# Performance work log

Measured on AMD Instinct MI355X. Metric: run time of the kernel, lower is better.

## Reference

```python
import jax, jax.numpy as jnp
import numpy as np


def _dequantize(qweight, scale, zero_point, bits, group_size):
    """Unpack int32-packed weights and apply group-wise dequantization.

    qweight:    [N, K // (32//bits)] int32, value i within an int32 at shift i*bits
    scale/zp:   [N, K // group_size]
    returns W:  [N, K] float32
    """
    vpi = 32 // bits  # values per int32
    mask = (1 << bits) - 1
    N, packed = qweight.shape
    K = packed * vpi
    shifts = (jnp.arange(vpi, dtype=jnp.int32) * bits)  # [vpi]
    # [N, packed, vpi] -> flatten so value i of each int32 lands at consecutive K positions
    q = (qweight[:, :, None] >> shifts[None, None, :]) & mask
    q = q.reshape(N, K // group_size, group_size).astype(jnp.float32)
    w = scale[:, :, None] * (q - zero_point[:, :, None])  # group-wise dequant
    return w.reshape(N, K)


def setup_inputs() -> dict:
    key = jax.random.key(0)
    k1, k2, k3, k4, k5 = jax.random.split(key, 5)
    B, S, K, N = 4, 2048, 4096, 4096
    bits, group_size = 4, 128
    vpi = 32 // bits
    num_groups = K // group_size
    x = jax.random.normal(k1, (B, S, K), dtype=jnp.float32)
    qweight = jax.random.randint(k2, (N, K // vpi), jnp.iinfo(jnp.int32).min,
                                 jnp.iinfo(jnp.int32).max, dtype=jnp.int32)
    scale = jax.random.uniform(k3, (N, num_groups), dtype=jnp.float32,
                               minval=0.001, maxval=0.02)
    zero_point = jax.random.uniform(k4, (N, num_groups), dtype=jnp.float32,
                                    minval=0.0, maxval=float((1 << bits) - 1))
    bias = jax.random.normal(k5, (N,), dtype=jnp.float32)
    return {"x": x, "qweight": qweight, "scale": scale, "zero_point": zero_point,
            "bias": bias, "bits": bits, "group_size": group_size}


def reference(x, qweight, scale, zero_point, bias, bits, group_size):
    # Fused dequant + GEMM: y = x @ W^T + b, W dequantized from packed int4 groups
    w = _dequantize(qweight, scale, zero_point, bits, group_size)  # [N, K]
    y = jnp.einsum('bsk,nk->bsn', x, w)
    return y + bias
```

## Files before the change

### kernel.cpp

```cpp
#include <hip/hip_runtime.h>

#define KD 4096
#define ND 4096
#define GRP 32

typedef unsigned short u16;
typedef float   f32x4  __attribute__((ext_vector_type(4)));
typedef __bf16  bf16x8 __attribute__((ext_vector_type(8)));
typedef unsigned short u16x8 __attribute__((ext_vector_type(8)));
typedef unsigned short u16x4 __attribute__((ext_vector_type(4)));

__device__ __forceinline__ u16 f2bf(float f) {
  unsigned u = __float_as_uint(f);
  return (u16)((u + 0x7fffu + ((u >> 16) & 1u)) >> 16);
}

__device__ __forceinline__ void async16(const void* g, void* l) {
  __builtin_amdgcn_global_load_lds(
      (const __attribute__((address_space(1))) unsigned int*)g,
      (__attribute__((address_space(3))) unsigned int*)l, 16, 0, 0);
}

__global__ __launch_bounds__(256) void prep_kernel(
    const int* __restrict__ qw, const float* __restrict__ scale,
    const float* __restrict__ zp, u16* __restrict__ wout,
    const float4* __restrict__ x, u16x4* __restrict__ xb) {
  const int b = blockIdx.x, tid = threadIdx.x;
  if (b < 8192) {
    int idx = b * 256 + tid;
    int n = idx >> 9;
    int p = idx & 511;
    int g = p >> 4;
    float s = scale[n * GRP + g];
    float bz = -s * zp[n * GRP + g];
    unsigned q = (unsigned)qw[idx];
    u16x8 hv;
#pragma unroll
    for (int i = 0; i < 8; ++i)
      hv[i] = f2bf(fmaf((float)((q >> (4 * i)) & 15u), s, bz));
    *(u16x8*)(wout + (size_t)idx * 8) = hv;
  } else {
    size_t i = (size_t)(b - 8192) * 256 + tid;
    float4 v = x[i];
    u16x4 h;
    h[0] = f2bf(v.x); h[1] = f2bf(v.y); h[2] = f2bf(v.z); h[3] = f2bf(v.w);
    xb[i] = h;
  }
}

template <int XF32, int WQ>
__global__ __launch_bounds__(256, 3) void gemm_kernel(
    const u16*   __restrict__ xb,
    const float* __restrict__ xf,
    const u16*   __restrict__ wb,
    const int*   __restrict__ qw,
    const float* __restrict__ scale,
    const float* __restrict__ zp,
    const float* __restrict__ bias,
    float* __restrict__ out) {
  __shared__ u16 As[128 * 64];
  __shared__ u16 Bs[128 * 64];
  const int tid = threadIdx.x;
  const int l = tid & 63, w = tid >> 6;
  const int m0 = blockIdx.y * 128, n0 = blockIdx.x * 128;
  const int wm = (w >> 1) * 64, wn = (w & 1) * 64;
  const int col = l & 15, quad = l >> 4;
  const int rsw = col & 7;
  const int lr = l >> 3;
  const int csrc = (l & 7) ^ lr;
  f32x4 acc[4][4] = {};

  for (int k0 = 0; k0 < KD; k0 += 64) {
    __syncthreads();

    if constexpr (XF32) {
#pragma unroll
      for (int it = 0; it < 8; ++it) {
        int fi = it * 256 + tid;
        int row = fi >> 4, cs = fi & 15;
        float4 v = *(const float4*)(xf + (size_t)(m0 + row) * KD + k0 + cs * 4);
        u16x4 h;
        h[0] = f2bf(v.x); h[1] = f2bf(v.y); h[2] = f2bf(v.z); h[3] = f2bf(v.w);
        int slot = (cs >> 1) ^ (row & 7);
        *(u16x4*)(&As[row * 64 + slot * 8 + (cs & 1) * 4]) = h;
      }
    } else {
#pragma unroll
      for (int c = 0; c < 4; ++c) {
        int br = w * 32 + c * 8;
        const u16* g = xb + (size_t)(m0 + br + lr) * KD + k0 + csrc * 8;
        async16(g, &As[br * 64]);
      }
    }

    if constexpr (WQ) {
#pragma unroll
      for (int it = 0; it < 4; ++it) {
        int qi = it * 256 + tid;
        int row = qi >> 3, p8 = qi & 7;
        int nrow = n0 + row;
        int g = k0 >> 7;
        float s = scale[nrow * GRP + g];
        float bz = -s * zp[nrow * GRP + g];
        unsigned q = (unsigned)qw[(size_t)nrow * (KD / 8) + (k0 >> 3) + p8];
        u16x8 hv;
#pragma unroll
        for (int i = 0; i < 8; ++i)
          hv[i] = f2bf(fmaf((float)((q >> (4 * i)) & 15u), s, bz));
        *(u16x8*)(&Bs[row * 64 + ((p8 ^ (row & 7)) * 8)]) = hv;
      }
    } else {
#pragma unroll
      for (int c = 0; c < 4; ++c) {
        int br = w * 32 + c * 8;
        const u16* g = wb + (size_t)(n0 + br + lr) * KD + k0 + csrc * 8;
        async16(g, &Bs[br * 64]);
      }
    }

    __syncthreads();

#pragma unroll
    for (int kk = 0; kk < 2; ++kk) {
      bf16x8 a[4], b[4];
      const int slot = ((kk * 4 + quad) ^ rsw) * 8;
#pragma unroll
      for (int i = 0; i < 4; ++i)
        a[i] = *(const bf16x8*)&As[(wm + i * 16 + col) * 64 + slot];
#pragma unroll
      for (int j = 0; j < 4; ++j)
        b[j] = *(const bf16x8*)&Bs[(wn + j * 16 + col) * 64 + slot];
#pragma unroll
      for (int i = 0; i < 4; ++i)
#pragma unroll
        for (int j = 0; j < 4; ++j)
          acc[i][j] = __builtin_amdgcn_mfma_f32_16x16x32_bf16(a[i], b[j], acc[i][j], 0, 0, 0);
    }
  }

#pragma unroll
  for (int j = 0; j < 4; ++j) {
    int n = n0 + wn + j * 16 + col;
    float bj = bias[n];
#pragma unroll
    for (int i = 0; i < 4; ++i) {
      int mrow = m0 + wm + i * 16 + quad * 4;
#pragma unroll
      for (int r = 0; r < 4; ++r)
        out[(size_t)(mrow + r) * ND + n] = acc[i][j][r] + bj;
    }
  }
}

extern "C" void kernel_launch(void* const* d_in, const int* in_sizes, int n_in,
                              void* d_out, int out_size, void* d_ws, size_t ws_size,
                              hipStream_t stream) {
  const float* x     = (const float*)d_in[0];
  const int*   qw    = (const int*)d_in[1];
  const float* scale = (const float*)d_in[2];
  const float* zp    = (const float*)d_in[3];
  const float* bias  = (const float*)d_in[4];
  float* out = (float*)d_out;

  const int M = in_sizes[0] / KD;
  dim3 grid(ND / 128, M / 128), block(256);

  const size_t needW = (size_t)ND * KD * sizeof(u16);
  const size_t needX = (size_t)M * KD * sizeof(u16);

  if (ws_size >= needW + needX) {
    u16* wb = (u16*)d_ws;
    u16* xb = wb + (size_t)ND * KD;
    int conv_blocks = (M * (KD / 4)) / 256;
    prep_kernel<<<8192 + conv_blocks, 256, 0, stream>>>(
        qw, scale, zp, wb, (const float4*)x, (u16x4*)xb);
    gemm_kernel<0, 0><<<grid, block, 0, stream>>>(xb, x, wb, qw, scale, zp, bias, out);
  } else if (ws_size >= needW) {
    u16* wb = (u16*)d_ws;
    prep_kernel<<<8192, 256, 0, stream>>>(qw, scale, zp, wb, nullptr, nullptr);
    gemm_kernel<1, 0><<<grid, block, 0, stream>>>(nullptr, x, wb, qw, scale, zp, bias, out);
  } else {
    gemm_kernel<1, 1><<<grid, block, 0, stream>>>(nullptr, x, nullptr, qw, scale, zp, bias, out);
  }
}
```

Baseline: 460.2 us.

## Add 256x256 double-buffered GEMM with XCD-aware block remap and grid-stride prep

```diff
diff --git a/kernel.cpp b/kernel.cpp
--- a/kernel.cpp
+++ b/kernel.cpp
@@ -3,6 +3,7 @@
 #define KD 4096
 #define ND 4096
 #define GRP 32
+#define NT (KD / 64)
 
 typedef unsigned short u16;
 typedef float   f32x4  __attribute__((ext_vector_type(4)));
@@ -24,10 +25,10 @@
 __global__ __launch_bounds__(256) void prep_kernel(
     const int* __restrict__ qw, const float* __restrict__ scale,
     const float* __restrict__ zp, u16* __restrict__ wout,
-    const float4* __restrict__ x, u16x4* __restrict__ xb) {
-  const int b = blockIdx.x, tid = threadIdx.x;
-  if (b < 8192) {
-    int idx = b * 256 + tid;
+    const float4* __restrict__ x, u16x4* __restrict__ xb, int nx) {
+  const int nth = gridDim.x * 256;
+  const int t0 = blockIdx.x * 256 + threadIdx.x;
+  for (int idx = t0; idx < ND * (KD / 8); idx += nth) {
     int n = idx >> 9;
     int p = idx & 511;
     int g = p >> 4;
@@ -39,8 +40,8 @@
     for (int i = 0; i < 8; ++i)
       hv[i] = f2bf(fmaf((float)((q >> (4 * i)) & 15u), s, bz));
     *(u16x8*)(wout + (size_t)idx * 8) = hv;
-  } else {
-    size_t i = (size_t)(b - 8192) * 256 + tid;
+  }
+  for (int i = t0; i < nx; i += nth) {
     float4 v = x[i];
     u16x4 h;
     h[0] = f2bf(v.x); h[1] = f2bf(v.y); h[2] = f2bf(v.z); h[3] = f2bf(v.w);
@@ -48,11 +49,156 @@
   }
 }
 
+__global__ __launch_bounds__(512, 2) void gemm256(
+    const u16* __restrict__ xb, const u16* __restrict__ wb,
+    const float* __restrict__ bias, float* __restrict__ out) {
+  __shared__ u16 As[2][256 * 64];
+  __shared__ u16 Bs[2][256 * 64];
+  const int tid = threadIdx.x;
+  const int l = tid & 63, w = tid >> 6;
+  const int wr = w >> 2, wc = w & 3;
+  const int col = l & 15, quad = l >> 4, rsw = col & 7;
+  const int lr = l >> 3, csrc = (l & 7) ^ lr;
+
+  const int id = blockIdx.y * gridDim.x + blockIdx.x;
+  const int nwg = gridDim.x * gridDim.y;
+  const int q = nwg >> 3, r = nwg & 7;
+  const int xcd = id & 7, off = id >> 3;
+  const int wgid = (xcd < r ? xcd * (q + 1) : r * (q + 1) + (xcd - r) * q) + off;
+  const int nb = gridDim.x;
+  const int m0 = (wgid / nb) * 256;
+  const int n0 = (wgid % nb) * 256;
+
+  const u16* asrc = xb + (size_t)(m0 + w * 16 + lr) * KD + csrc * 8;
+  const u16* bsrc = wb + (size_t)(n0 + w * 16 + lr) * KD + csrc * 8;
+
+#define STAGE_A(t, h)                                                      \
+  do {                                                                     \
+    const u16* _g = asrc + (size_t)((h) * 128) * KD + (t) * 64;            \
+    u16* _l = &As[(t) & 1][((h) * 128 + w * 16) * 64];                     \
+    async16(_g, _l);                                                       \
+    async16(_g + (size_t)8 * KD, _l + 8 * 64);                             \
+  } while (0)
+#define STAGE_B(t, h)                                                      \
+  do {                                                                     \
+    const u16* _g = bsrc + (size_t)((h) * 128) * KD + (t) * 64;            \
+    u16* _l = &Bs[(t) & 1][((h) * 128 + w * 16) * 64];                     \
+    async16(_g, _l);                                                       \
+    async16(_g + (size_t)8 * KD, _l + 8 * 64);                             \
+  } while (0)
+#define BAR()    asm volatile("s_barrier" ::: "memory")
+#define LGKM0()  asm volatile("s_waitcnt lgkmcnt(0)" ::: "memory")
+#define VMCNT2() asm volatile("s_waitcnt vmcnt(2)" ::: "memory")
+#define VMCNT0() asm volatile("s_waitcnt vmcnt(0)" ::: "memory")
+#define LDA(Ab, i, kk) \
+  (*(const bf16x8*)&(Ab)[(wr * 128 + (i) * 16 + col) * 64 + ((((kk) * 4 + quad) ^ rsw) * 8)])
+#define LDB(Bb, j, kk) \
+  (*(const bf16x8*)&(Bb)[(wc * 64 + (j) * 16 + col) * 64 + ((((kk) * 4 + quad) ^ rsw) * 8)])
+
+  f32x4 acc[8][4] = {};
+  bf16x8 a[4][2], b[4][2];
+
+  STAGE_A(0, 0); STAGE_A(0, 1); STAGE_B(0, 0); STAGE_B(0, 1);
+  STAGE_A(1, 0);
+  VMCNT2();
+  BAR();
+
+  for (int t = 0; t < NT; ++t) {
+    const u16* Ab = As[t & 1];
+    const u16* Bb = Bs[t & 1];
+
+#pragma unroll
+    for (int i = 0; i < 4; ++i) { a[i][0] = LDA(Ab, i, 0); a[i][1] = LDA(Ab, i, 1); }
+#pragma unroll
+    for (int j = 0; j < 2; ++j) { b[j][0] = LDB(Bb, j, 0); b[j][1] = LDB(Bb, j, 1); }
+    if (t + 1 < NT) STAGE_A(t + 1, 1);
+    BAR();
+    LGKM0();
+    __builtin_amdgcn_s_setprio(1);
+#pragma unroll
+    for (int kk = 0; kk < 2; ++kk)
+#pragma unroll
+      for (int i = 0; i < 4; ++i)
+#pragma unroll
+        for (int j = 0; j < 2; ++j)
+          acc[i][j] = __builtin_amdgcn_mfma_f32_16x16x32_bf16(a[i][kk], b[j][kk], acc[i][j], 0, 0, 0);
+    __builtin_amdgcn_s_setprio(0);
+    BAR();
+
+#pragma unroll
+    for (int j = 2; j < 4; ++j) { b[j][0] = LDB(Bb, j, 0); b[j][1] = LDB(Bb, j, 1); }
+    if (t + 1 < NT) STAGE_B(t + 1, 0);
+    BAR();
+    LGKM0();
+    __builtin_amdgcn_s_setprio(1);
+#pragma unroll
+    for (int kk = 0; kk < 2; ++kk)
+#pragma unroll
+      for (int i = 0; i < 4; ++i)
+#pragma unroll
+        for (int j = 2; j < 4; ++j)
+          acc[i][j] = __builtin_amdgcn_mfma_f32_16x16x32_bf16(a[i][kk], b[j][kk], acc[i][j], 0, 0, 0);
+    __builtin_amdgcn_s_setprio(0);
+    BAR();
+
+#pragma unroll
+    for (int i = 0; i < 4; ++i) { a[i][0] = LDA(Ab, i + 4, 0); a[i][1] = LDA(Ab, i + 4, 1); }
+    if (t + 1 < NT) STAGE_B(t + 1, 1);
+    BAR();
+    LGKM0();
+    __builtin_amdgcn_s_setprio(1);
+#pragma unroll
+    for (int kk = 0; kk < 2; ++kk)
+#pragma unroll
+      for (int i = 0; i < 4; ++i)
+#pragma unroll
+        for (int j = 0; j < 2; ++j)
+          acc[4 + i][j] = __builtin_amdgcn_mfma_f32_16x16x32_bf16(a[i][kk], b[j][kk], acc[4 + i][j], 0, 0, 0);
+    __builtin_amdgcn_s_setprio(0);
+    BAR();
+
+    if (t + 2 < NT) STAGE_A(t + 2, 0);
+    BAR();
+    __builtin_amdgcn_s_setprio(1);
+#pragma unroll
+    for (int kk = 0; kk < 2; ++kk)
+#pragma unroll
+      for (int i = 0; i < 4; ++i)
+#pragma unroll
+        for (int j = 2; j < 4; ++j)
+          acc[4 + i][j] = __builtin_amdgcn_mfma_f32_16x16x32_bf16(a[i][kk], b[j][kk], acc[4 + i][j], 0, 0, 0);
+    __builtin_amdgcn_s_setprio(0);
+    if (t + 2 < NT) VMCNT2(); else VMCNT0();
+    BAR();
+  }
+
+#pragma unroll
+  for (int j = 0; j < 4; ++j) {
+    int n = n0 + wc * 64 + j * 16 + col;
+    float bj = bias[n];
+#pragma unroll
+    for (int i = 0; i < 8; ++i) {
+      int mrow = m0 + wr * 128 + i * 16 + quad * 4;
+#pragma unroll
+      for (int rr = 0; rr < 4; ++rr)
+        out[(size_t)(mrow + rr) * ND + n] = acc[i][j][rr] + bj;
+    }
+  }
+#undef STAGE_A
+#undef STAGE_B
+#undef BAR
+#undef LGKM0
+#undef VMCNT2
+#undef VMCNT0
+#undef LDA
+#undef LDB
+}
+
 template <int XF32, int WQ>
 __global__ __launch_bounds__(256, 3) void gemm_kernel(
-    const u16*   __restrict__ xb,
+    const u16*   __restrict__ xbp,
     const float* __restrict__ xf,
-    const u16*   __restrict__ wb,
+    const u16*   __restrict__ wbp,
     const int*   __restrict__ qw,
     const float* __restrict__ scale,
     const float* __restrict__ zp,
@@ -88,7 +234,7 @@
 #pragma unroll
       for (int c = 0; c < 4; ++c) {
         int br = w * 32 + c * 8;
-        const u16* g = xb + (size_t)(m0 + br + lr) * KD + k0 + csrc * 8;
+        const u16* g = xbp + (size_t)(m0 + br + lr) * KD + k0 + csrc * 8;
         async16(g, &As[br * 64]);
       }
     }
@@ -102,18 +248,18 @@
         int g = k0 >> 7;
         float s = scale[nrow * GRP + g];
         float bz = -s * zp[nrow * GRP + g];
-        unsigned q = (unsigned)qw[(size_t)nrow * (KD / 8) + (k0 >> 3) + p8];
+        unsigned qv = (unsigned)qw[(size_t)nrow * (KD / 8) + (k0 >> 3) + p8];
         u16x8 hv;
 #pragma unroll
         for (int i = 0; i < 8; ++i)
-          hv[i] = f2bf(fmaf((float)((q >> (4 * i)) & 15u), s, bz));
+          hv[i] = f2bf(fmaf((float)((qv >> (4 * i)) & 15u), s, bz));
         *(u16x8*)(&Bs[row * 64 + ((p8 ^ (row & 7)) * 8)]) = hv;
       }
     } else {
 #pragma unroll
       for (int c = 0; c < 4; ++c) {
         int br = w * 32 + c * 8;
-        const u16* g = wb + (size_t)(n0 + br + lr) * KD + k0 + csrc * 8;
+        const u16* g = wbp + (size_t)(n0 + br + lr) * KD + k0 + csrc * 8;
         async16(g, &Bs[br * 64]);
       }
     }
@@ -146,8 +292,8 @@
     for (int i = 0; i < 4; ++i) {
       int mrow = m0 + wm + i * 16 + quad * 4;
 #pragma unroll
-      for (int r = 0; r < 4; ++r)
-        out[(size_t)(mrow + r) * ND + n] = acc[i][j][r] + bj;
+      for (int rr = 0; rr < 4; ++rr)
+        out[(size_t)(mrow + rr) * ND + n] = acc[i][j][rr] + bj;
     }
   }
 }
@@ -163,23 +309,25 @@
   float* out = (float*)d_out;
 
   const int M = in_sizes[0] / KD;
-  dim3 grid(ND / 128, M / 128), block(256);
 
   const size_t needW = (size_t)ND * KD * sizeof(u16);
   const size_t needX = (size_t)M * KD * sizeof(u16);
 
-  if (ws_size >= needW + needX) {
+  if (ws_size >= needW + needX && (M % 256) == 0) {
     u16* wb = (u16*)d_ws;
-    u16* xb = wb + (size_t)ND * KD;
-    int conv_blocks = (M * (KD / 4)) / 256;
-    prep_kernel<<<8192 + conv_blocks, 256, 0, stream>>>(
-        qw, scale, zp, wb, (const float4*)x, (u16x4*)xb);
-    gemm_kernel<0, 0><<<grid, block, 0, stream>>>(xb, x, wb, qw, scale, zp, bias, out);
+    u16* xbuf = wb + (size_t)ND * KD;
+    prep_kernel<<<2048, 256, 0, stream>>>(qw, scale, zp, wb,
+                                          (const float4*)x, (u16x4*)xbuf,
+                                          M * (KD / 4));
+    dim3 grid(ND / 256, M / 256);
+    gemm256<<<grid, dim3(512), 0, stream>>>(xbuf, wb, bias, out);
   } else if (ws_size >= needW) {
     u16* wb = (u16*)d_ws;
-    prep_kernel<<<8192, 256, 0, stream>>>(qw, scale, zp, wb, nullptr, nullptr);
-    gemm_kernel<1, 0><<<grid, block, 0, stream>>>(nullptr, x, wb, qw, scale, zp, bias, out);
+    prep_kernel<<<2048, 256, 0, stream>>>(qw, scale, zp, wb, nullptr, nullptr, 0);
+    dim3 grid(ND / 128, M / 128);
+    gemm_kernel<1, 0><<<grid, dim3(256), 0, stream>>>(nullptr, x, wb, qw, scale, zp, bias, out);
   } else {
-    gemm_kernel<1, 1><<<grid, block, 0, stream>>>(nullptr, x, nullptr, qw, scale, zp, bias, out);
-  }
-}
+    dim3 grid(ND / 128, M / 128);
+    gemm_kernel<1, 1><<<grid, dim3(256), 0, stream>>>(nullptr, x, nullptr, qw, scale, zp, bias, out);
+  }
+}
```

New measurement: 499.3 us. 1.09x slower.
